# Performance work log

Measured on AMD Instinct MI355X. Metric: run time of the kernel, lower is better.

## Reference

```python
import jax, jax.numpy as jnp
import numpy as np

IMAGE_SIZE = 800.0          # torchvision default min_size
SCORE_THRESH = 0.25         # box_score_thresh from __init__
NMS_THRESH = 0.5            # box_nms_thresh from __init__
MAX_DET = 100               # torchvision detections_per_img default
BBOX_XFORM_CLIP = float(np.log(1000.0 / 16.0))  # torchvision BoxCoder clamp


def setup_inputs() -> dict:
    key = jax.random.key(0)
    k = jax.random.split(key, 5)
    B, N, D, C = 16, 4000, 1024, 2
    feats = jax.random.normal(k[0], (B, N, D), dtype=jnp.float32)
    # valid proposal boxes (x1,y1,x2,y2) inside the image
    cxcy = jax.random.uniform(k[1], (B, N, 2), minval=64.0, maxval=IMAGE_SIZE - 64.0)
    wh = jax.random.uniform(k[2], (B, N, 2), minval=16.0, maxval=128.0)
    proposals = jnp.concatenate([cxcy - wh * 0.5, cxcy + wh * 0.5], axis=-1)
    W_cls = jax.random.normal(k[3], (C, D), dtype=jnp.float32) * 0.02
    b_cls = jnp.zeros((C,), jnp.float32)
    W_box = jax.random.normal(k[4], (C * 4, D), dtype=jnp.float32) * 0.01
    b_box = jnp.zeros((C * 4,), jnp.float32)
    return dict(feats=feats, proposals=proposals, W_cls=W_cls, b_cls=b_cls,
                W_box=W_box, b_box=b_box)


def _decode_boxes(deltas, proposals):
    # torchvision BoxCoder with weights (10, 10, 5, 5)
    wx, wy, ww, wh = 10.0, 10.0, 5.0, 5.0
    widths = proposals[..., 2] - proposals[..., 0]
    heights = proposals[..., 3] - proposals[..., 1]
    ctr_x = proposals[..., 0] + 0.5 * widths
    ctr_y = proposals[..., 1] + 0.5 * heights
    dx = deltas[..., 0] / wx
    dy = deltas[..., 1] / wy
    dw = jnp.minimum(deltas[..., 2] / ww, BBOX_XFORM_CLIP)
    dh = jnp.minimum(deltas[..., 3] / wh, BBOX_XFORM_CLIP)
    pcx = dx * widths + ctr_x
    pcy = dy * heights + ctr_y
    pw = jnp.exp(dw) * widths
    ph = jnp.exp(dh) * heights
    boxes = jnp.stack([pcx - 0.5 * pw, pcy - 0.5 * ph,
                       pcx + 0.5 * pw, pcy + 0.5 * ph], axis=-1)
    return jnp.clip(boxes, 0.0, IMAGE_SIZE)


def _nms_keep(boxes, scores):
    # greedy NMS for one image; boxes [N,4], scores [N] (already thresholded)
    areas = jnp.maximum(boxes[:, 2] - boxes[:, 0], 0.0) * \
            jnp.maximum(boxes[:, 3] - boxes[:, 1], 0.0)

    def body(carry, _):
        s, keep = carry
        i = jnp.argmax(s)
        valid = s[i] > 0.0
        bi = boxes[i]
        ix1 = jnp.maximum(bi[0], boxes[:, 0])
        iy1 = jnp.maximum(bi[1], boxes[:, 1])
        ix2 = jnp.minimum(bi[2], boxes[:, 2])
        iy2 = jnp.minimum(bi[3], boxes[:, 3])
        inter = jnp.maximum(ix2 - ix1, 0.0) * jnp.maximum(iy2 - iy1, 0.0)
        iou = inter / (areas[i] + areas - inter + 1e-9)
        s = jnp.where(iou > NMS_THRESH, 0.0, s).at[i].set(0.0)
        keep = keep.at[i].set(valid)
        return (s, keep), None

    init = (scores, jnp.zeros(scores.shape, dtype=bool))
    (_, keep), _ = jax.lax.scan(body, init, None, length=MAX_DET)
    return keep


def reference(feats, proposals, W_cls, b_cls, W_box, b_box):
    logits = jnp.einsum('bnd,cd->bnc', feats, W_cls) + b_cls       # [B,N,2]
    deltas = jnp.einsum('bnd,ed->bne', feats, W_box) + b_box       # [B,N,8]
    probs = jax.nn.softmax(logits, axis=-1)
    scores = probs[..., 1]                                          # foreground class
    fg_deltas = deltas[..., 4:8]                                    # class-1 deltas
    boxes = _decode_boxes(fg_deltas, proposals)                     # [B,N,4]
    scores = jnp.where(scores > SCORE_THRESH, scores, 0.0)
    keep = jax.vmap(_nms_keep)(boxes, scores)                       # [B,N] bool
    final_scores = scores * keep.astype(scores.dtype)
    return jnp.concatenate([boxes, final_scores[..., None]], axis=-1)  # [B,N,5]
```

## Files before the change

### kernel.cpp

```cpp
#include <hip/hip_runtime.h>
#include <math.h>

#define IMG 800.0f
#define SCORE_TH 0.25f
#define NMS_TH 0.5f
#define MAXDET 100
#define BBOX_CLIP 4.135166556742356f

constexpr int kB = 16;
constexpr int kN = 4000;
constexpr int kD = 1024;

__global__ __launch_bounds__(256, 2) void head_kernel(
    const float* __restrict__ feats, const float* __restrict__ proposals,
    const float* __restrict__ Wc, const float* __restrict__ bc,
    const float* __restrict__ Wb, const float* __restrict__ bb,
    float* __restrict__ out, float* __restrict__ ws_scores,
    float* __restrict__ ws_boxes) {
  const int lane = threadIdx.x & 63;
  const int waveId = (blockIdx.x * blockDim.x + threadIdx.x) >> 6;
  const int nWaves = (gridDim.x * blockDim.x) >> 6;

  const float4* Wc4 = (const float4*)Wc;
  const float4* Wb4 = (const float4*)Wb;
  float4 w0[4], w1[4], w4[4], w5[4], w6[4], w7[4];
#pragma unroll
  for (int ch = 0; ch < 4; ++ch) {
    int idx = ch * 64 + lane;
    w0[ch] = Wc4[0 * 256 + idx];
    w1[ch] = Wc4[1 * 256 + idx];
    w4[ch] = Wb4[4 * 256 + idx];
    w5[ch] = Wb4[5 * 256 + idx];
    w6[ch] = Wb4[6 * 256 + idx];
    w7[ch] = Wb4[7 * 256 + idx];
  }
  const float bc0 = bc[0], bc1 = bc[1];
  const float bb4 = bb[4], bb5 = bb[5], bb6 = bb[6], bb7 = bb[7];

  const int R = kB * kN;
  for (int row = waveId; row < R; row += nWaves) {
    const float4* F = (const float4*)(feats + (size_t)row * kD);
    float a0 = 0.f, a1 = 0.f, a4 = 0.f, a5 = 0.f, a6 = 0.f, a7 = 0.f;
#pragma unroll
    for (int ch = 0; ch < 4; ++ch) {
      float4 f = F[ch * 64 + lane];
      a0 = fmaf(f.x, w0[ch].x, fmaf(f.y, w0[ch].y, fmaf(f.z, w0[ch].z, fmaf(f.w, w0[ch].w, a0))));
      a1 = fmaf(f.x, w1[ch].x, fmaf(f.y, w1[ch].y, fmaf(f.z, w1[ch].z, fmaf(f.w, w1[ch].w, a1))));
      a4 = fmaf(f.x, w4[ch].x, fmaf(f.y, w4[ch].y, fmaf(f.z, w4[ch].z, fmaf(f.w, w4[ch].w, a4))));
      a5 = fmaf(f.x, w5[ch].x, fmaf(f.y, w5[ch].y, fmaf(f.z, w5[ch].z, fmaf(f.w, w5[ch].w, a5))));
      a6 = fmaf(f.x, w6[ch].x, fmaf(f.y, w6[ch].y, fmaf(f.z, w6[ch].z, fmaf(f.w, w6[ch].w, a6))));
      a7 = fmaf(f.x, w7[ch].x, fmaf(f.y, w7[ch].y, fmaf(f.z, w7[ch].z, fmaf(f.w, w7[ch].w, a7))));
    }
#pragma unroll
    for (int off = 32; off; off >>= 1) {
      a0 += __shfl_xor(a0, off);
      a1 += __shfl_xor(a1, off);
      a4 += __shfl_xor(a4, off);
      a5 += __shfl_xor(a5, off);
      a6 += __shfl_xor(a6, off);
      a7 += __shfl_xor(a7, off);
    }
    if (lane == 0) {
      float l0 = a0 + bc0, l1 = a1 + bc1;
      float score = 1.0f / (1.0f + __expf(l0 - l1));
      float sth = score > SCORE_TH ? score : 0.0f;

      float4 p = ((const float4*)proposals)[row];
      float w = p.z - p.x, h = p.w - p.y;
      float cx = p.x + 0.5f * w, cy = p.y + 0.5f * h;
      float dx = (a4 + bb4) * 0.1f;
      float dy = (a5 + bb5) * 0.1f;
      float dw = fminf((a6 + bb6) * 0.2f, BBOX_CLIP);
      float dh = fminf((a7 + bb7) * 0.2f, BBOX_CLIP);
      float pcx = fmaf(dx, w, cx), pcy = fmaf(dy, h, cy);
      float pw = __expf(dw) * w, ph = __expf(dh) * h;
      float x1 = fminf(fmaxf(pcx - 0.5f * pw, 0.f), IMG);
      float y1 = fminf(fmaxf(pcy - 0.5f * ph, 0.f), IMG);
      float x2 = fminf(fmaxf(pcx + 0.5f * pw, 0.f), IMG);
      float y2 = fminf(fmaxf(pcy + 0.5f * ph, 0.f), IMG);

      size_t ob = (size_t)row * 5;
      out[ob + 0] = x1;
      out[ob + 1] = y1;
      out[ob + 2] = x2;
      out[ob + 3] = y2;
      ws_scores[row] = sth;
      ((float4*)ws_boxes)[row] = make_float4(x1, y1, x2, y2);
    }
  }
}

__global__ __launch_bounds__(256, 1) void nms_kernel(
    const float* __restrict__ ws_scores, const float* __restrict__ ws_boxes,
    float* __restrict__ out) {
  const int b = blockIdx.x;
  const int t = threadIdx.x;
  const int wave = t >> 6;
  const int lane = t & 63;

  __shared__ float4 Lbox[kN];
  __shared__ float Lval[2][4];
  __shared__ int Lidx[2][4];

  const float* sc = ws_scores + (size_t)b * kN;
  const float4* bx = (const float4*)ws_boxes + (size_t)b * kN;

  float s[16], areaE[16];
  float4 box[16];
  unsigned keep_mask = 0u;

#pragma unroll
  for (int k = 0; k < 16; ++k) {
    int n = k * 256 + t;
    if (n < kN) {
      box[k] = bx[n];
      s[k] = sc[n];
      areaE[k] = fmaxf(box[k].z - box[k].x, 0.f) *
                     fmaxf(box[k].w - box[k].y, 0.f) +
                 1e-9f;
      Lbox[n] = box[k];
    } else {
      box[k] = make_float4(0.f, 0.f, 0.f, 0.f);
      s[k] = -1.0f;
      areaE[k] = 1e-9f;
    }
  }

  {
    float bv = s[0];
    int bi = t;
#pragma unroll
    for (int k = 1; k < 16; ++k)
      if (s[k] > bv) { bv = s[k]; bi = k * 256 + t; }
#pragma unroll
    for (int off = 32; off; off >>= 1) {
      float ov = __shfl_xor(bv, off);
      int oi = __shfl_xor(bi, off);
      if (ov > bv || (ov == bv && oi < bi)) { bv = ov; bi = oi; }
    }
    if (lane == 0) { Lval[1][wave] = bv; Lidx[1][wave] = bi; }
  }
  __syncthreads();

  for (int it = 0; it < MAXDET; ++it) {
    const int pr = (it + 1) & 1;
    float wv = Lval[pr][0];
    int wi = Lidx[pr][0];
#pragma unroll
    for (int w = 1; w < 4; ++w) {
      float ov = Lval[pr][w];
      int oi = Lidx[pr][w];
      if (ov > wv || (ov == wv && oi < wi)) { wv = ov; wi = oi; }
    }
    const bool valid = wv > 0.0f;
    const float4 wb = Lbox[wi];
    const float wa = fmaxf(wb.z - wb.x, 0.f) * fmaxf(wb.w - wb.y, 0.f);
    const bool iOwn = (t == (wi & 255));
    const int oSlot = wi >> 8;
    const float2 wb_lo = make_float2(wb.x, wb.y);
    const float2 wb_hi = make_float2(wb.z, wb.w);

    float bv;
    int bi;
#pragma unroll
    for (int k = 0; k < 16; ++k) {
      float2 lo, hi, d;
      lo.x = fmaxf(wb_lo.x, box[k].x);
      lo.y = fmaxf(wb_lo.y, box[k].y);
      hi.x = fminf(wb_hi.x, box[k].z);
      hi.y = fminf(wb_hi.y, box[k].w);
      d.x = hi.x - lo.x;
      d.y = hi.y - lo.y;
      float inter = fmaxf(d.x, 0.f) * fmaxf(d.y, 0.f);
      float denom = wa + areaE[k] - inter;
      bool sup = inter > 0.5f * denom;
      bool sel = iOwn && (k == oSlot);
      if (sel)
        keep_mask = valid ? (keep_mask | (1u << k)) : (keep_mask & ~(1u << k));
      if (sup | sel) s[k] = 0.0f;
      if (k == 0) {
        bv = s[0];
        bi = t;
      } else if (s[k] > bv) {
        bv = s[k];
        bi = k * 256 + t;
      }
    }
#pragma unroll
    for (int off = 32; off; off >>= 1) {
      float ov = __shfl_xor(bv, off);
      int oi = __shfl_xor(bi, off);
      if (ov > bv || (ov == bv && oi < bi)) { bv = ov; bi = oi; }
    }
    if (lane == 0) { Lval[it & 1][wave] = bv; Lidx[it & 1][wave] = bi; }
    __syncthreads();
  }

#pragma unroll
  for (int k = 0; k < 16; ++k) {
    int n = k * 256 + t;
    if (n < kN) {
      out[((size_t)(b * kN + n)) * 5 + 4] =
          (keep_mask >> k) & 1u ? sc[n] : 0.0f;
    }
  }
}

extern "C" void kernel_launch(void* const* d_in, const int* in_sizes, int n_in,
                              void* d_out, int out_size, void* d_ws,
                              size_t ws_size, hipStream_t stream) {
  const float* feats = (const float*)d_in[0];
  const float* proposals = (const float*)d_in[1];
  const float* Wc = (const float*)d_in[2];
  const float* bc = (const float*)d_in[3];
  const float* Wb = (const float*)d_in[4];
  const float* bb = (const float*)d_in[5];
  float* out = (float*)d_out;

  float* ws_scores = (float*)d_ws;
  float* ws_boxes = ws_scores + kB * kN;

  head_kernel<<<512, 256, 0, stream>>>(feats, proposals, Wc, bc, Wb, bb, out,
                                       ws_scores, ws_boxes);
  nms_kernel<<<kB, 256, 0, stream>>>(ws_scores, ws_boxes, out);
}
```

Before: 526.1 us.

## Pack score and index into u64 keys and reduce argmax with DPP

The NMS argmax now packs each score's float bits with an inverted index into one 64-bit key. Each thread reduces its slots with a tree of max operations and each wave reduces with DPP row and broadcast ops, replacing the paired float/int shuffle-xor butterfly. The IoU test is rewritten as 3*inter > areaA+areaB, which drops the subtraction and a multiply, and the keep-mask update is hoisted out of the per-slot loop. The aim is to shorten the serial critical path of each of the 100 NMS iterations. Using scores as unsigned bits relies on them being non-negative, and the rewritten IoU comparison can differ slightly in rounding.

```diff
diff --git a/kernel.cpp b/kernel.cpp
--- a/kernel.cpp
+++ b/kernel.cpp
@@ -90,6 +90,25 @@
   }
 }
 
+template <int CTRL>
+__device__ __forceinline__ unsigned long long dpp_max_u64(unsigned long long k) {
+  int lo = __builtin_amdgcn_update_dpp(0, (int)(unsigned)k, CTRL, 0xF, 0xF, true);
+  int hi =
+      __builtin_amdgcn_update_dpp(0, (int)(unsigned)(k >> 32), CTRL, 0xF, 0xF, true);
+  unsigned long long o = ((unsigned long long)(unsigned)hi << 32) | (unsigned)lo;
+  return o > k ? o : k;
+}
+
+__device__ __forceinline__ unsigned long long wave_max_u64(unsigned long long k) {
+  k = dpp_max_u64<0x121>(k);
+  k = dpp_max_u64<0x122>(k);
+  k = dpp_max_u64<0x124>(k);
+  k = dpp_max_u64<0x128>(k);
+  k = dpp_max_u64<0x142>(k);
+  k = dpp_max_u64<0x143>(k);
+  return k;
+}
+
 __global__ __launch_bounds__(256, 1) void nms_kernel(
     const float* __restrict__ ws_scores, const float* __restrict__ ws_boxes,
     float* __restrict__ out) {
@@ -99,100 +118,84 @@
   const int lane = t & 63;
 
   __shared__ float4 Lbox[kN];
-  __shared__ float Lval[2][4];
-  __shared__ int Lidx[2][4];
+  __shared__ unsigned long long Lkey[2][4];
 
   const float* sc = ws_scores + (size_t)b * kN;
   const float4* bx = (const float4*)ws_boxes + (size_t)b * kN;
 
-  float s[16], areaE[16];
+  unsigned khi[16];
+  float areaE[16];
   float4 box[16];
   unsigned keep_mask = 0u;
+  const unsigned nt = ~(unsigned)t;
 
 #pragma unroll
   for (int k = 0; k < 16; ++k) {
     int n = k * 256 + t;
     if (n < kN) {
       box[k] = bx[n];
-      s[k] = sc[n];
+      khi[k] = __float_as_uint(sc[n]);
       areaE[k] = fmaxf(box[k].z - box[k].x, 0.f) *
                      fmaxf(box[k].w - box[k].y, 0.f) +
                  1e-9f;
       Lbox[n] = box[k];
     } else {
       box[k] = make_float4(0.f, 0.f, 0.f, 0.f);
-      s[k] = -1.0f;
+      khi[k] = 0u;
       areaE[k] = 1e-9f;
     }
   }
 
-  {
-    float bv = s[0];
-    int bi = t;
-#pragma unroll
-    for (int k = 1; k < 16; ++k)
-      if (s[k] > bv) { bv = s[k]; bi = k * 256 + t; }
-#pragma unroll
-    for (int off = 32; off; off >>= 1) {
-      float ov = __shfl_xor(bv, off);
-      int oi = __shfl_xor(bi, off);
-      if (ov > bv || (ov == bv && oi < bi)) { bv = ov; bi = oi; }
-    }
-    if (lane == 0) { Lval[1][wave] = bv; Lidx[1][wave] = bi; }
-  }
+  auto reduce_publish = [&](int parity) {
+    unsigned long long lk[16];
+#pragma unroll
+    for (int k = 0; k < 16; ++k)
+      lk[k] = ((unsigned long long)khi[k] << 32) |
+              (unsigned long long)(nt - (unsigned)(k * 256));
+#pragma unroll
+    for (int k = 0; k < 8; ++k) lk[k] = lk[k] > lk[k + 8] ? lk[k] : lk[k + 8];
+#pragma unroll
+    for (int k = 0; k < 4; ++k) lk[k] = lk[k] > lk[k + 4] ? lk[k] : lk[k + 4];
+    lk[0] = lk[0] > lk[2] ? lk[0] : lk[2];
+    lk[1] = lk[1] > lk[3] ? lk[1] : lk[3];
+    lk[0] = lk[0] > lk[1] ? lk[0] : lk[1];
+    unsigned long long wkey = wave_max_u64(lk[0]);
+    if (lane == 63) Lkey[parity][wave] = wkey;
+  };
+
+  reduce_publish(1);
   __syncthreads();
 
   for (int it = 0; it < MAXDET; ++it) {
     const int pr = (it + 1) & 1;
-    float wv = Lval[pr][0];
-    int wi = Lidx[pr][0];
-#pragma unroll
-    for (int w = 1; w < 4; ++w) {
-      float ov = Lval[pr][w];
-      int oi = Lidx[pr][w];
-      if (ov > wv || (ov == wv && oi < wi)) { wv = ov; wi = oi; }
-    }
-    const bool valid = wv > 0.0f;
-    const float4 wb = Lbox[wi];
+    unsigned long long wk = Lkey[pr][0];
+    unsigned long long k1 = Lkey[pr][1];
+    unsigned long long k2 = Lkey[pr][2];
+    unsigned long long k3 = Lkey[pr][3];
+    wk = wk > k1 ? wk : k1;
+    k2 = k2 > k3 ? k2 : k3;
+    wk = wk > k2 ? wk : k2;
+    const unsigned whi = (unsigned)__builtin_amdgcn_readfirstlane((int)(wk >> 32));
+    const unsigned wlo = (unsigned)__builtin_amdgcn_readfirstlane((int)(unsigned)wk);
+    const unsigned wn = ~wlo;
+    const bool valid = whi != 0u;
+    const float4 wb = Lbox[wn];
     const float wa = fmaxf(wb.z - wb.x, 0.f) * fmaxf(wb.w - wb.y, 0.f);
-    const bool iOwn = (t == (wi & 255));
-    const int oSlot = wi >> 8;
-    const float2 wb_lo = make_float2(wb.x, wb.y);
-    const float2 wb_hi = make_float2(wb.z, wb.w);
-
-    float bv;
-    int bi;
+    const bool iOwn = ((unsigned)t == (wn & 255u));
+    const int oSlot = (int)(wn >> 8);
+    if (iOwn) {
+      unsigned bit = 1u << oSlot;
+      keep_mask = valid ? (keep_mask | bit) : (keep_mask & ~bit);
+    }
 #pragma unroll
     for (int k = 0; k < 16; ++k) {
-      float2 lo, hi, d;
-      lo.x = fmaxf(wb_lo.x, box[k].x);
-      lo.y = fmaxf(wb_lo.y, box[k].y);
-      hi.x = fminf(wb_hi.x, box[k].z);
-      hi.y = fminf(wb_hi.y, box[k].w);
-      d.x = hi.x - lo.x;
-      d.y = hi.y - lo.y;
-      float inter = fmaxf(d.x, 0.f) * fmaxf(d.y, 0.f);
-      float denom = wa + areaE[k] - inter;
-      bool sup = inter > 0.5f * denom;
-      bool sel = iOwn && (k == oSlot);
-      if (sel)
-        keep_mask = valid ? (keep_mask | (1u << k)) : (keep_mask & ~(1u << k));
-      if (sup | sel) s[k] = 0.0f;
-      if (k == 0) {
-        bv = s[0];
-        bi = t;
-      } else if (s[k] > bv) {
-        bv = s[k];
-        bi = k * 256 + t;
-      }
-    }
-#pragma unroll
-    for (int off = 32; off; off >>= 1) {
-      float ov = __shfl_xor(bv, off);
-      int oi = __shfl_xor(bi, off);
-      if (ov > bv || (ov == bv && oi < bi)) { bv = ov; bi = oi; }
-    }
-    if (lane == 0) { Lval[it & 1][wave] = bv; Lidx[it & 1][wave] = bi; }
+      float dx = fminf(wb.z, box[k].z) - fmaxf(wb.x, box[k].x);
+      float dy = fminf(wb.w, box[k].w) - fmaxf(wb.y, box[k].y);
+      float inter3 = 3.0f * fmaxf(dx, 0.f) * fmaxf(dy, 0.f);
+      bool sup = inter3 > wa + areaE[k];
+      if (sup || (iOwn && k == oSlot)) khi[k] = 0u;
+    }
+    reduce_publish(it & 1);
     __syncthreads();
   }
 
```

Measured after the change: 444.6 us. -15.5%, faster.
